# Kernel tuning notes

Measured on AMD Instinct MI355X. Metric: run time of the kernel, lower is better.

Reference implementation:

```python
import jax, jax.numpy as jnp
import numpy as np

N = 100000   # total nodes in batch
E = 1600000  # directed edges
G = 512      # graphs in batch
D_IN = 128
H = 128      # hidden_dim
L = 5        # num GIN layers
BN_EPS = 1e-5


def _bn(x, p):
    # p: [4, d] = (gamma, beta, running_mean, running_var); eval-mode batchnorm
    g, b, m, v = p[0], p[1], p[2], p[3]
    return (x - m) * jax.lax.rsqrt(v + BN_EPS) * g + b


def _mk_bn(k, d):
    k1, k2, k3, k4 = jax.random.split(k, 4)
    return jnp.stack([
        jax.random.uniform(k1, (d,), minval=0.8, maxval=1.2),
        0.1 * jax.random.normal(k2, (d,)),
        0.1 * jax.random.normal(k3, (d,)),
        jax.random.uniform(k4, (d,), minval=0.5, maxval=1.5),
    ])


def _mk_w(k, fi, fo):
    return jax.random.normal(k, (fi, fo)) * (2.0 / (fi + fo)) ** 0.5


def setup_inputs() -> dict:
    key = jax.random.key(0)
    ks = iter(jax.random.split(key, 64))
    nk = lambda: next(ks)

    x = jax.random.normal(nk(), (N, D_IN), dtype=jnp.float32)
    edge_index = jax.random.randint(nk(), (2, E), 0, N, dtype=jnp.int32)
    batch = jnp.sort(jax.random.randint(nk(), (N,), 0, G, dtype=jnp.int32))

    in_W = _mk_w(nk(), D_IN, H); in_b = jnp.zeros((H,)); in_bn = _mk_bn(nk(), H)

    W1, b1, bn1, W2, b2, bn2, W3, b3, nbn = [], [], [], [], [], [], [], [], []
    for _ in range(L):
        W1.append(_mk_w(nk(), H, 3 * H)); b1.append(jnp.zeros((3 * H,))); bn1.append(_mk_bn(nk(), 3 * H))
        W2.append(_mk_w(nk(), 3 * H, 2 * H)); b2.append(jnp.zeros((2 * H,))); bn2.append(_mk_bn(nk(), 2 * H))
        W3.append(_mk_w(nk(), 2 * H, H)); b3.append(jnp.zeros((H,)))
        nbn.append(_mk_bn(nk(), H))
    stk = lambda xs: jnp.stack(xs)
    eps_g = 0.1 * jax.random.normal(nk(), (L,))

    cls_W1 = _mk_w(nk(), 3 * H, H); cls_b1 = jnp.zeros((H,)); cls_bn1 = _mk_bn(nk(), H)
    cls_W2 = _mk_w(nk(), H, H // 2); cls_b2 = jnp.zeros((H // 2,)); cls_bn2 = _mk_bn(nk(), H // 2)
    fin_W = _mk_w(nk(), H // 2, 6); fin_b = jnp.zeros((6,))

    return {
        "x": x, "edge_index": edge_index, "batch": batch,
        "in_W": in_W, "in_b": in_b, "in_bn": in_bn,
        "W1": stk(W1), "b1": stk(b1), "bn1": stk(bn1),
        "W2": stk(W2), "b2": stk(b2), "bn2": stk(bn2),
        "W3": stk(W3), "b3": stk(b3), "eps_g": eps_g, "node_bn": stk(nbn),
        "cls_W1": cls_W1, "cls_b1": cls_b1, "cls_bn1": cls_bn1,
        "cls_W2": cls_W2, "cls_b2": cls_b2, "cls_bn2": cls_bn2,
        "fin_W": fin_W, "fin_b": fin_b,
    }


def reference(x, edge_index, batch, in_W, in_b, in_bn, W1, b1, bn1, W2, b2, bn2,
              W3, b3, eps_g, node_bn, cls_W1, cls_b1, cls_bn1, cls_W2, cls_b2,
              cls_bn2, fin_W, fin_b):
    src, dst = edge_index[0], edge_index[1]
    # input projection (dropout is identity in eval mode)
    h = jax.nn.relu(_bn(x @ in_W + in_b, in_bn))  # [N, H]

    for i in range(L):
        # GINConv: (1 + eps) * x + sum over in-neighbors, then MLP
        agg = jax.ops.segment_sum(h[src], dst, num_segments=N)  # [N, H]
        z = (1.0 + eps_g[i]) * h + agg
        z = jax.nn.relu(_bn(z @ W1[i] + b1[i], bn1[i]))
        z = jax.nn.relu(_bn(z @ W2[i] + b2[i], bn2[i]))
        z = z @ W3[i] + b3[i]
        # node-level BatchNorm + ReLU after conv
        z = jax.nn.relu(_bn(z, node_bn[i]))
        h = z if i == 0 else h + z  # residual for i > 0

    # multi-pool readout: add / mean / max over graphs
    s = jax.ops.segment_sum(h, batch, num_segments=G)          # [G, H]
    cnt = jax.ops.segment_sum(jnp.ones((N,), h.dtype), batch, num_segments=G)
    mean = s / jnp.maximum(cnt, 1.0)[:, None]
    mx = jax.ops.segment_max(h, batch, num_segments=G)
    mx = jnp.where(cnt[:, None] > 0, mx, 0.0)
    g = jnp.concatenate([s, mean, mx], axis=1)                 # [G, 3H]

    f = jax.nn.relu(_bn(g @ cls_W1 + cls_b1, cls_bn1))
    f = jax.nn.relu(_bn(f @ cls_W2 + cls_b2, cls_bn2))
    logits = f @ fin_W + fin_b                                  # [G, 6]
    return logits
```

## Files before the change

kernel.cpp:

```cpp
#include <hip/hip_runtime.h>
#include <hip/hip_bf16.h>

#define GLOBAL_AS __attribute__((address_space(1)))
#define LDS_AS    __attribute__((address_space(3)))

typedef __attribute__((ext_vector_type(4))) float  f32x4;
typedef __attribute__((ext_vector_type(8))) short  bf16x8;

static constexpr int   H      = 128;
static constexpr float BN_EPS = 1e-5f;

__device__ __forceinline__ float bf2f(ushort u) {
  union { unsigned u; float f; } x; x.u = ((unsigned)u) << 16; return x.f;
}
__device__ __forceinline__ ushort f2bf(float f) {
  union { float f; unsigned u; } x; x.f = f;
  unsigned r = x.u + 0x7fffu + ((x.u >> 16) & 1u);
  return (ushort)(r >> 16);
}

__device__ __forceinline__ void fold_pack_one(const float* __restrict__ W,
                                              const float* __restrict__ b,
                                              const float* __restrict__ bn,
                                              int K, int NOUT, int idx,
                                              ushort* __restrict__ Wp,
                                              float* __restrict__ bout) {
  int o = idx / K, k = idx - o * K;
  float scale = 1.0f, shift = 0.0f;
  if (bn != nullptr) {
    float g = bn[o], be = bn[NOUT + o], m = bn[2 * NOUT + o], v = bn[3 * NOUT + o];
    scale = g * rsqrtf(v + BN_EPS);
    shift = be - m * scale;
  }
  int gt = o >> 4, lr = o & 15, ks = k >> 5, lk = (k >> 3) & 3, e = k & 7;
  size_t pos = ((((size_t)gt * (K / 32) + ks) * 64) + lk * 16 + lr) * 8 + e;
  Wp[pos] = f2bf(W[(size_t)k * NOUT + o] * scale);
  if (k == 0) bout[o] = b[o] * scale + shift;
}

__device__ __forceinline__ void fold_f32_one(const float* __restrict__ W,
                                             const float* __restrict__ b,
                                             const float* __restrict__ bn,
                                             int K, int NOUT, int idx,
                                             float* __restrict__ Wt,
                                             float* __restrict__ bout) {
  int o = idx / K, k = idx - o * K;
  float scale = 1.0f, shift = 0.0f;
  if (bn != nullptr) {
    float g = bn[o], be = bn[NOUT + o], m = bn[2 * NOUT + o], v = bn[3 * NOUT + o];
    scale = g * rsqrtf(v + BN_EPS);
    shift = be - m * scale;
  }
  Wt[(size_t)o * K + k] = W[(size_t)k * NOUT + o] * scale;
  if (k == 0) bout[o] = b[o] * scale + shift;
}

__global__ __launch_bounds__(256) void fold_all_kernel(
    const float* __restrict__ in_W, const float* __restrict__ in_b, const float* __restrict__ in_bn,
    const float* __restrict__ W1, const float* __restrict__ b1, const float* __restrict__ bn1,
    const float* __restrict__ W2, const float* __restrict__ b2, const float* __restrict__ bn2,
    const float* __restrict__ W3, const float* __restrict__ b3, const float* __restrict__ nbn,
    const float* __restrict__ cW1, const float* __restrict__ cb1, const float* __restrict__ cbn1,
    const float* __restrict__ cW2, const float* __restrict__ cb2, const float* __restrict__ cbn2,
    const float* __restrict__ fW, const float* __restrict__ fb,
    ushort* __restrict__ wIn, float* __restrict__ bIn,
    ushort* __restrict__ w1f, float* __restrict__ b1f,
    ushort* __restrict__ w2f, float* __restrict__ b2f,
    ushort* __restrict__ w3f, float* __restrict__ b3f,
    float* __restrict__ cw1f, float* __restrict__ cb1f,
    float* __restrict__ cw2f, float* __restrict__ cb2f,
    float* __restrict__ cw3f, float* __restrict__ cb3f) {
  int idx = blockIdx.x * 256 + threadIdx.x;
  if (idx < 16384) {
    fold_pack_one(in_W, in_b, in_bn, 128, 128, idx, wIn, bIn);
    return;
  }
  idx -= 16384;
  if (idx < 5 * 180224) {
    int layer = idx / 180224;
    int r = idx - layer * 180224;
    if (r < 49152) {
      fold_pack_one(W1 + (size_t)layer * 49152, b1 + (size_t)layer * 384,
                    bn1 + (size_t)layer * 4 * 384, 128, 384, r,
                    w1f + (size_t)layer * 49152, b1f + (size_t)layer * 384);
    } else if (r < 147456) {
      fold_pack_one(W2 + (size_t)layer * 98304, b2 + (size_t)layer * 256,
                    bn2 + (size_t)layer * 4 * 256, 384, 256, r - 49152,
                    w2f + (size_t)layer * 98304, b2f + (size_t)layer * 256);
    } else {
      fold_pack_one(W3 + (size_t)layer * 32768, b3 + (size_t)layer * 128,
                    nbn + (size_t)layer * 4 * 128, 256, 128, r - 147456,
                    w3f + (size_t)layer * 32768, b3f + (size_t)layer * 128);
    }
    return;
  }
  idx -= 5 * 180224;
  if (idx < 49152) { fold_f32_one(cW1, cb1, cbn1, 384, 128, idx, cw1f, cb1f); return; }
  idx -= 49152;
  if (idx < 8192)  { fold_f32_one(cW2, cb2, cbn2, 128, 64, idx, cw2f, cb2f); return; }
  idx -= 8192;
  if (idx < 384)   { fold_f32_one(fW, fb, nullptr, 64, 6, idx, cw3f, cb3f); return; }
}

__global__ void cvt4_kernel(const float* __restrict__ x, ushort* __restrict__ xb, int n4) {
  int i = blockIdx.x * blockDim.x + threadIdx.x;
  if (i >= n4) return;
  float4 v = ((const float4*)x)[i];
  ushort4 o; o.x = f2bf(v.x); o.y = f2bf(v.y); o.z = f2bf(v.z); o.w = f2bf(v.w);
  ((ushort4*)xb)[i] = o;
}

__global__ void hist_kernel(const int* __restrict__ idx, int n, int* __restrict__ cnt) {
  int i = blockIdx.x * blockDim.x + threadIdx.x;
  if (i < n) atomicAdd(&cnt[idx[i]], 1);
}

__global__ void gbound_kernel(const int* __restrict__ batch, int N, int G,
                              int* __restrict__ gptr) {
  int i = blockIdx.x * blockDim.x + threadIdx.x;
  if (i >= N) return;
  int b = batch[i];
  int prev = (i == 0) ? -1 : batch[i - 1];
  for (int g = prev + 1; g <= b; ++g) gptr[g] = i;
  if (i == N - 1) for (int g = b + 1; g <= G; ++g) gptr[g] = N;
}

__global__ void block_sum_kernel(const int* __restrict__ v, int n, int* __restrict__ bsum) {
  __shared__ int s[256];
  int i = blockIdx.x * 256 + threadIdx.x;
  int x = (i < n) ? v[i] : 0;
  s[threadIdx.x] = x; __syncthreads();
  for (int off = 128; off > 0; off >>= 1) {
    if (threadIdx.x < (unsigned)off) s[threadIdx.x] += s[threadIdx.x + off];
    __syncthreads();
  }
  if (threadIdx.x == 0) bsum[blockIdx.x] = s[0];
}

__global__ void scan_block_kernel(int* __restrict__ bsum, int nb,
                                  int* __restrict__ last_out, int total) {
  __shared__ int s[256];
  __shared__ int carry;
  if (threadIdx.x == 0) carry = 0;
  __syncthreads();
  for (int base = 0; base < nb; base += 256) {
    int i = base + threadIdx.x;
    int x = (i < nb) ? bsum[i] : 0;
    s[threadIdx.x] = x; __syncthreads();
    for (int off = 1; off < 256; off <<= 1) {
      int add = (threadIdx.x >= (unsigned)off) ? s[threadIdx.x - off] : 0;
      __syncthreads();
      s[threadIdx.x] += add;
      __syncthreads();
    }
    if (i < nb) bsum[i] = carry + s[threadIdx.x] - x;
    __syncthreads();
    if (threadIdx.x == 0) carry += s[255];
    __syncthreads();
  }
  if (last_out && threadIdx.x == 0) *last_out = total;
}

__global__ void scan_final_kernel(const int* __restrict__ v, int n, const int* __restrict__ bsum,
                                  int* __restrict__ rowptr, int* __restrict__ cursor) {
  __shared__ int s[256];
  int i = blockIdx.x * 256 + threadIdx.x;
  int x = (i < n) ? v[i] : 0;
  s[threadIdx.x] = x; __syncthreads();
  for (int off = 1; off < 256; off <<= 1) {
    int add = (threadIdx.x >= (unsigned)off) ? s[threadIdx.x - off] : 0;
    __syncthreads();
    s[threadIdx.x] += add;
    __syncthreads();
  }
  if (i < n) {
    int excl = bsum[blockIdx.x] + s[threadIdx.x] - x;
    rowptr[i] = excl;
    if (cursor) cursor[i] = excl;
  }
}

__global__ __launch_bounds__(256) void scatter_part_kernel(
    const int* __restrict__ src, const int* __restrict__ dst, int E,
    int* __restrict__ cursor, int* __restrict__ col, int npp) {
  const int part  = blockIdx.x & 7;
  const int chunk = blockIdx.x >> 3;
  const int lo = part * npp, hi = lo + npp;
  const int i0 = chunk * 1024 + threadIdx.x * 4;
  if (i0 + 3 < E) {
    int4 d4 = *(const int4*)(dst + i0);
    if (d4.x >= lo && d4.x < hi) { int p = atomicAdd(&cursor[d4.x], 1); col[p] = src[i0 + 0]; }
    if (d4.y >= lo && d4.y < hi) { int p = atomicAdd(&cursor[d4.y], 1); col[p] = src[i0 + 1]; }
    if (d4.z >= lo && d4.z < hi) { int p = atomicAdd(&cursor[d4.z], 1); col[p] = src[i0 + 2]; }
    if (d4.w >= lo && d4.w < hi) { int p = atomicAdd(&cursor[d4.w], 1); col[p] = src[i0 + 3]; }
  } else {
    for (int u = 0; u < 4; ++u) {
      int i = i0 + u;
      if (i < E) {
        int d = dst[i];
        if (d >= lo && d < hi) { int p = atomicAdd(&cursor[d], 1); col[p] = src[i]; }
      }
    }
  }
}

__global__ __launch_bounds__(256) void agg_kernel(
    const ushort* __restrict__ hb,
    const int* __restrict__ rowptr, const int* __restrict__ col,
    const float* __restrict__ eps_g, int layer,
    ushort* __restrict__ z, int n) {
  int node = blockIdx.x * 4 + (threadIdx.x >> 6);
  if (node >= n) return;
  const int lane = threadIdx.x & 63;
  const int l16  = lane & 15;
  const int grp  = lane >> 4;
  const int s = rowptr[node], e = rowptr[node + 1];
  float a0 = 0.f, a1 = 0.f, a2 = 0.f, a3 = 0.f, a4 = 0.f, a5 = 0.f, a6 = 0.f, a7 = 0.f;
  const size_t co = (size_t)l16 * 8;
  int j = s + grp;
  for (; j + 12 < e; j += 16) {
    int i0 = col[j], i1 = col[j + 4], i2 = col[j + 8], i3 = col[j + 12];
    bf16x8 v0 = *(const bf16x8*)(hb + (size_t)i0 * H + co);
    bf16x8 v1 = *(const bf16x8*)(hb + (size_t)i1 * H + co);
    bf16x8 v2 = *(const bf16x8*)(hb + (size_t)i2 * H + co);
    bf16x8 v3 = *(const bf16x8*)(hb + (size_t)i3 * H + co);
    a0 += (bf2f((ushort)v0[0]) + bf2f((ushort)v1[0])) + (bf2f((ushort)v2[0]) + bf2f((ushort)v3[0]));
    a1 += (bf2f((ushort)v0[1]) + bf2f((ushort)v1[1])) + (bf2f((ushort)v2[1]) + bf2f((ushort)v3[1]));
    a2 += (bf2f((ushort)v0[2]) + bf2f((ushort)v1[2])) + (bf2f((ushort)v2[2]) + bf2f((ushort)v3[2]));
    a3 += (bf2f((ushort)v0[3]) + bf2f((ushort)v1[3])) + (bf2f((ushort)v2[3]) + bf2f((ushort)v3[3]));
    a4 += (bf2f((ushort)v0[4]) + bf2f((ushort)v1[4])) + (bf2f((ushort)v2[4]) + bf2f((ushort)v3[4]));
    a5 += (bf2f((ushort)v0[5]) + bf2f((ushort)v1[5])) + (bf2f((ushort)v2[5]) + bf2f((ushort)v3[5]));
    a6 += (bf2f((ushort)v0[6]) + bf2f((ushort)v1[6])) + (bf2f((ushort)v2[6]) + bf2f((ushort)v3[6]));
    a7 += (bf2f((ushort)v0[7]) + bf2f((ushort)v1[7])) + (bf2f((ushort)v2[7]) + bf2f((ushort)v3[7]));
  }
  for (; j + 4 < e; j += 8) {
    int i0 = col[j], i1 = col[j + 4];
    bf16x8 v0 = *(const bf16x8*)(hb + (size_t)i0 * H + co);
    bf16x8 v1 = *(const bf16x8*)(hb + (size_t)i1 * H + co);
    a0 += bf2f((ushort)v0[0]) + bf2f((ushort)v1[0]);
    a1 += bf2f((ushort)v0[1]) + bf2f((ushort)v1[1]);
    a2 += bf2f((ushort)v0[2]) + bf2f((ushort)v1[2]);
    a3 += bf2f((ushort)v0[3]) + bf2f((ushort)v1[3]);
    a4 += bf2f((ushort)v0[4]) + bf2f((ushort)v1[4]);
    a5 += bf2f((ushort)v0[5]) + bf2f((ushort)v1[5]);
    a6 += bf2f((ushort)v0[6]) + bf2f((ushort)v1[6]);
    a7 += bf2f((ushort)v0[7]) + bf2f((ushort)v1[7]);
  }
  if (j < e) {
    bf16x8 v0 = *(const bf16x8*)(hb + (size_t)col[j] * H + co);
    a0 += bf2f((ushort)v0[0]); a1 += bf2f((ushort)v0[1]);
    a2 += bf2f((ushort)v0[2]); a3 += bf2f((ushort)v0[3]);
    a4 += bf2f((ushort)v0[4]); a5 += bf2f((ushort)v0[5]);
    a6 += bf2f((ushort)v0[6]); a7 += bf2f((ushort)v0[7]);
  }
  a0 += __shfl_xor(a0, 16); a0 += __shfl_xor(a0, 32);
  a1 += __shfl_xor(a1, 16); a1 += __shfl_xor(a1, 32);
  a2 += __shfl_xor(a2, 16); a2 += __shfl_xor(a2, 32);
  a3 += __shfl_xor(a3, 16); a3 += __shfl_xor(a3, 32);
  a4 += __shfl_xor(a4, 16); a4 += __shfl_xor(a4, 32);
  a5 += __shfl_xor(a5, 16); a5 += __shfl_xor(a5, 32);
  a6 += __shfl_xor(a6, 16); a6 += __shfl_xor(a6, 32);
  a7 += __shfl_xor(a7, 16); a7 += __shfl_xor(a7, 32);
  float sx, sy;
  if      (grp == 0) { sx = a0; sy = a1; }
  else if (grp == 1) { sx = a2; sy = a3; }
  else if (grp == 2) { sx = a4; sy = a5; }
  else               { sx = a6; sy = a7; }
  const int c0 = l16 * 8 + grp * 2;
  float ep = 1.0f + eps_g[layer];
  ushort2 hs = *(const ushort2*)(hb + (size_t)node * H + c0);
  ushort2 o;
  o.x = f2bf(ep * bf2f(hs.x) + sx);
  o.y = f2bf(ep * bf2f(hs.y) + sy);
  *(ushort2*)(z + (size_t)node * H + c0) = o;
}

template<int K, int NOUT>
__global__ __launch_bounds__(256) void gemm_kernel(
    const ushort* __restrict__ A, const ushort* __restrict__ Wp,
    const float* __restrict__ bias,
    ushort* __restrict__ outb, float* __restrict__ hf) {
  constexpr int ROWB = 2 * K;
  __shared__ __align__(16) char lds[64 * ROWB];
  const int t = threadIdx.x;
  const long row0 = (long)blockIdx.x * 64;
  const char* Ab = (const char*)(A + (size_t)row0 * K);

  constexpr int ITERS = (64 * ROWB) / (256 * 16);
#pragma unroll
  for (int it = 0; it < ITERS; ++it) {
    int ob = (it * 256 + t) * 16;
    int r = ob / ROWB;
    int c = ob - r * ROWB;
    int sb = r * ROWB + (c ^ ((r & 7) << 4));
    __builtin_amdgcn_global_load_lds((const GLOBAL_AS void*)(Ab + sb),
                                     (LDS_AS void*)(lds + ob), 16, 0, 0);
  }
  __syncthreads();

  const int l  = t & 63;
  const int w  = t >> 6;
  const int lr = l & 15;
  const int lk = l >> 4;
  constexpr int CPW = NOUT / 4;
  constexpr int NCT = CPW / 16;

  for (int ct = 0; ct < NCT; ++ct) {
    const int colbase = w * CPW + ct * 16;
    const ushort* tb = Wp + ((size_t)(colbase >> 4) * (K / 32)) * 512;
    f32x4 acc[4] = {};
#pragma unroll
    for (int ks = 0; ks < K / 32; ++ks) {
      bf16x8 bfr = *(const bf16x8*)(tb + ks * 512 + l * 8);
#pragma unroll
      for (int rt = 0; rt < 4; ++rt) {
        const int rr = rt * 16 + lr;
        const int kb = ks * 64 + lk * 16;
        bf16x8 afr = *(const bf16x8*)(lds + rr * ROWB + (kb ^ ((rr & 7) << 4)));
        acc[rt] = __builtin_amdgcn_mfma_f32_16x16x32_bf16(bfr, afr, acc[rt], 0, 0, 0);
      }
    }
    const int c0 = colbase + lk * 4;
    const float b0 = bias[c0], b1 = bias[c0 + 1], b2 = bias[c0 + 2], b3 = bias[c0 + 3];
#pragma unroll
    for (int rt = 0; rt < 4; ++rt) {
      const long grow = row0 + rt * 16 + lr;
      float v0 = fmaxf(acc[rt][0] + b0, 0.f);
      float v1 = fmaxf(acc[rt][1] + b1, 0.f);
      float v2 = fmaxf(acc[rt][2] + b2, 0.f);
      float v3 = fmaxf(acc[rt][3] + b3, 0.f);
      *(float4*)(hf + grow * H + c0) = make_float4(v0, v1, v2, v3);
      ushort4 sv; sv.x = f2bf(v0); sv.y = f2bf(v1); sv.z = f2bf(v2); sv.w = f2bf(v3);
      *(ushort4*)(outb + grow * NOUT + c0) = sv;
    }
  }
}

template<int HMODE>
__global__ __launch_bounds__(256, 4) void mlp_fused_kernel(
    const ushort* __restrict__ zin,
    const ushort* __restrict__ w1, const float* __restrict__ bb1,
    const ushort* __restrict__ w2, const float* __restrict__ bb2,
    const ushort* __restrict__ w3, const float* __restrict__ bb3,
    ushort* __restrict__ hb, float* __restrict__ hf) {
  __shared__ __align__(16) char lds[40 * 1024];
  char* t1 = lds;
  char* zz = lds + 24 * 1024;
  char* t2 = lds + 24 * 1024;

  const int t = threadIdx.x;
  const long row0 = (long)blockIdx.x * 32;
  const char* Ab = (const char*)(zin + (size_t)row0 * 128);

#pragma unroll
  for (int it = 0; it < 2; ++it) {
    int ob = (it * 256 + t) * 16;
    int r = ob >> 8;
    int c = ob & 255;
    int sb = r * 256 + (c ^ ((r & 7) << 4));
    __builtin_amdgcn_global_load_lds((const GLOBAL_AS void*)(Ab + sb),
                                     (LDS_AS void*)(zz + ob), 16, 0, 0);
  }
  __syncthreads();

  const int l  = t & 63;
  const int w  = t >> 6;
  const int lr = l & 15;
  const int lk = l >> 4;

#pragma unroll
  for (int pass = 0; pass < 2; ++pass) {
    const int cb0 = w * 96 + pass * 48;
    f32x4 acc[3][2] = {};
#pragma unroll
    for (int ks = 0; ks < 4; ++ks) {
      bf16x8 afr[2];
#pragma unroll
      for (int rt = 0; rt < 2; ++rt) {
        const int rr = rt * 16 + lr;
        afr[rt] = *(const bf16x8*)(zz + rr * 256 + ((ks * 64 + lk * 16) ^ ((rr & 7) << 4)));
      }
#pragma unroll
      for (int ct = 0; ct < 3; ++ct) {
        bf16x8 bfr = *(const bf16x8*)(w1 + ((size_t)(cb0 / 16 + ct) * 4 + ks) * 512 + l * 8);
#pragma unroll
        for (int rt = 0; rt < 2; ++rt)
          acc[ct][rt] = __builtin_amdgcn_mfma_f32_16x16x32_bf16(bfr, afr[rt], acc[ct][rt], 0, 0, 0);
      }
    }
#pragma unroll
    for (int ct = 0; ct < 3; ++ct) {
      const int c0 = cb0 + ct * 16 + lk * 4;
      const float b0 = bb1[c0], b1 = bb1[c0 + 1], b2 = bb1[c0 + 2], b3 = bb1[c0 + 3];
#pragma unroll
      for (int rt = 0; rt < 2; ++rt) {
        const int rr = rt * 16 + lr;
        ushort4 sv;
        sv.x = f2bf(fmaxf(acc[ct][rt][0] + b0, 0.f));
        sv.y = f2bf(fmaxf(acc[ct][rt][1] + b1, 0.f));
        sv.z = f2bf(fmaxf(acc[ct][rt][2] + b2, 0.f));
        sv.w = f2bf(fmaxf(acc[ct][rt][3] + b3, 0.f));
        *(ushort4*)(t1 + rr * 768 + ((c0 * 2) ^ ((rr & 7) << 4))) = sv;
      }
    }
  }
  __syncthreads();

  {
    f32x4 acc[4][2] = {};
#pragma unroll
    for (int ks = 0; ks < 12; ++ks) {
      bf16x8 afr[2];
#pragma unroll
      for (int rt = 0; rt < 2; ++rt) {
        const int rr = rt * 16 + lr;
        afr[rt] = *(const bf16x8*)(t1 + rr * 768 + ((ks * 64 + lk * 16) ^ ((rr & 7) << 4)));
      }
#pragma unroll
      for (int ct = 0; ct < 4; ++ct) {
        bf16x8 bfr = *(const bf16x8*)(w2 + ((size_t)(w * 4 + ct) * 12 + ks) * 512 + l * 8);
#pragma unroll
        for (int rt = 0; rt < 2; ++rt)
          acc[ct][rt] = __builtin_amdgcn_mfma_f32_16x16x32_bf16(bfr, afr[rt], acc[ct][rt], 0, 0, 0);
      }
    }
    __syncthreads();
#pragma unroll
    for (int ct = 0; ct < 4; ++ct) {
      const int c0 = w * 64 + ct * 16 + lk * 4;
      const float b0 = bb2[c0], b1 = bb2[c0 + 1], b2 = bb2[c0 + 2], b3 = bb2[c0 + 3];
#pragma unroll
      for (int rt = 0; rt < 2; ++rt) {
        const int rr = rt * 16 + lr;
        ushort4 sv;
        sv.x = f2bf(fmaxf(acc[ct][rt][0] + b0, 0.f));
        sv.y = f2bf(fmaxf(acc[ct][rt][1] + b1, 0.f));
        sv.z = f2bf(fmaxf(acc[ct][rt][2] + b2, 0.f));
        sv.w = f2bf(fmaxf(acc[ct][rt][3] + b3, 0.f));
        *(ushort4*)(t2 + rr * 512 + ((c0 * 2) ^ ((rr & 7) << 4))) = sv;
      }
    }
  }
  __syncthreads();

  {
    f32x4 acc[2][2] = {};
#pragma unroll
    for (int ks = 0; ks < 8; ++ks) {
      bf16x8 afr[2];
#pragma unroll
      for (int rt = 0; rt < 2; ++rt) {
        const int rr = rt * 16 + lr;
        afr[rt] = *(const bf16x8*)(t2 + rr * 512 + ((ks * 64 + lk * 16) ^ ((rr & 7) << 4)));
      }
#pragma unroll
      for (int ct = 0; ct < 2; ++ct) {
        bf16x8 bfr = *(const bf16x8*)(w3 + ((size_t)(w * 2 + ct) * 8 + ks) * 512 + l * 8);
#pragma unroll
        for (int rt = 0; rt < 2; ++rt)
          acc[ct][rt] = __builtin_amdgcn_mfma_f32_16x16x32_bf16(bfr, afr[rt], acc[ct][rt], 0, 0, 0);
      }
    }
#pragma unroll
    for (int ct = 0; ct < 2; ++ct) {
      const int c0 = w * 32 + ct * 16 + lk * 4;
      const float b0 = bb3[c0], b1 = bb3[c0 + 1], b2 = bb3[c0 + 2], b3v = bb3[c0 + 3];
#pragma unroll
      for (int rt = 0; rt < 2; ++rt) {
        const long grow = row0 + rt * 16 + lr;
        float v0 = fmaxf(acc[ct][rt][0] + b0, 0.f);
        float v1 = fmaxf(acc[ct][rt][1] + b1, 0.f);
        float v2 = fmaxf(acc[ct][rt][2] + b2, 0.f);
        float v3 = fmaxf(acc[ct][rt][3] + b3v, 0.f);
        float4* hp = (float4*)(hf + grow * H + c0);
        if (HMODE == 2) {
          float4 o = *hp;
          v0 += o.x; v1 += o.y; v2 += o.z; v3 += o.w;
        }
        *hp = make_float4(v0, v1, v2, v3);
        ushort4 sv; sv.x = f2bf(v0); sv.y = f2bf(v1); sv.z = f2bf(v2); sv.w = f2bf(v3);
        *(ushort4*)(hb + grow * H + c0) = sv;
      }
    }
  }
}

__global__ __launch_bounds__(128) void readout_kernel(const float* __restrict__ hf,
                                                      const int* __restrict__ gptr,
                                                      float* __restrict__ g) {
  int gi = blockIdx.x, t = threadIdx.x;
  int s = gptr[gi], e = gptr[gi + 1];
  float sum = 0.f, mx = -INFINITY;
  for (int n = s; n < e; ++n) {
    float v = hf[(size_t)n * H + t];
    sum += v; mx = fmaxf(mx, v);
  }
  int cnt = e - s;
  g[gi * 384 + t]       = sum;
  g[gi * 384 + 128 + t] = sum / fmaxf((float)cnt, 1.f);
  g[gi * 384 + 256 + t] = (cnt > 0) ? mx : 0.f;
}

__global__ __launch_bounds__(128) void classifier_kernel(
    const float* __restrict__ g,
    const float* __restrict__ W1, const float* __restrict__ b1,
    const float* __restrict__ W2, const float* __restrict__ b2,
    const float* __restrict__ W3, const float* __restrict__ b3,
    float* __restrict__ out) {
  __shared__ float row[384];
  __shared__ float f1[128];
  __shared__ float f2s[64];
  int gi = blockIdx.x, t = threadIdx.x;
  for (int i = t; i < 384; i += 128) row[i] = g[gi * 384 + i];
  __syncthreads();
  float a = b1[t];
  for (int k = 0; k < 384; ++k) a += row[k] * W1[t * 384 + k];
  f1[t] = fmaxf(a, 0.f);
  __syncthreads();
  if (t < 64) {
    float a2 = b2[t];
    for (int k = 0; k < 128; ++k) a2 += f1[k] * W2[t * 128 + k];
    f2s[t] = fmaxf(a2, 0.f);
  }
  __syncthreads();
  if (t < 6) {
    float a3 = b3[t];
    for (int k = 0; k < 64; ++k) a3 += f2s[k] * W3[t * 64 + k];
    out[gi * 6 + t] = a3;
  }
}

extern "C" void kernel_launch(void* const* d_in, const int* in_sizes, int n_in,
                              void* d_out, int out_size, void* d_ws, size_t ws_size,
                              hipStream_t stream) {
  (void)n_in; (void)ws_size;
  const float* x     = (const float*)d_in[0];
  const int*   eidx  = (const int*)d_in[1];
  const int*   batch = (const int*)d_in[2];
  const float* in_W  = (const float*)d_in[3];
  const float* in_b  = (const float*)d_in[4];
  const float* in_bn = (const float*)d_in[5];
  const float* W1    = (const float*)d_in[6];
  const float* b1    = (const float*)d_in[7];
  const float* bn1   = (const float*)d_in[8];
  const float* W2    = (const float*)d_in[9];
  const float* b2    = (const float*)d_in[10];
  const float* bn2   = (const float*)d_in[11];
  const float* W3    = (const float*)d_in[12];
  const float* b3    = (const float*)d_in[13];
  const float* eps_g = (const float*)d_in[14];
  const float* nbn   = (const float*)d_in[15];
  const float* cW1   = (const float*)d_in[16];
  const float* cb1   = (const float*)d_in[17];
  const float* cbn1  = (const float*)d_in[18];
  const float* cW2   = (const float*)d_in[19];
  const float* cb2   = (const float*)d_in[20];
  const float* cbn2  = (const float*)d_in[21];
  const float* fW    = (const float*)d_in[22];
  const float* fb    = (const float*)d_in[23];

  const int N  = in_sizes[0] / 128;
  const int E  = in_sizes[1] / 2;
  const int G  = out_size / 6;
  const int Mp = ((N + 63) / 64) * 64;
  const int gblocks = Mp / 64;
  const int mblocks = Mp / 32;
  const int npp = (N + 7) / 8;
  const int nchunks = (E + 1023) / 1024;

  char* p = (char*)d_ws;
  auto alloc = [&](size_t bytes) -> char* {
    char* r = p; p += (bytes + 255) & ~(size_t)255; return r;
  };
  ushort* hb     = (ushort*)alloc((size_t)Mp * H * 2);
  ushort* zb     = (ushort*)alloc((size_t)Mp * H * 2);
  ushort* xb     = (ushort*)alloc((size_t)Mp * H * 2);
  float*  hf     = (float*)alloc((size_t)Mp * H * 4);
  int*    deg    = (int*)alloc((size_t)N * 4);
  int*    rowptr = (int*)alloc((size_t)(N + 1) * 4);
  int*    cursor = (int*)alloc((size_t)N * 4);
  int*    colx   = (int*)alloc((size_t)E * 4);
  int*    bsum   = (int*)alloc(4096);
  int*    gptr   = (int*)alloc((size_t)(G + 1) * 4);
  float*  gbuf   = (float*)alloc((size_t)G * 384 * 4);
  ushort* wIn    = (ushort*)alloc(128 * 128 * 2);
  float*  bIn    = (float*)alloc(128 * 4);
  ushort* w1f    = (ushort*)alloc((size_t)5 * 384 * 128 * 2);
  float*  b1f    = (float*)alloc((size_t)5 * 384 * 4);
  ushort* w2f    = (ushort*)alloc((size_t)5 * 256 * 384 * 2);
  float*  b2f    = (float*)alloc((size_t)5 * 256 * 4);
  ushort* w3f    = (ushort*)alloc((size_t)5 * 128 * 256 * 2);
  float*  b3f    = (float*)alloc((size_t)5 * 128 * 4);
  float*  cw1f   = (float*)alloc(128 * 384 * 4);
  float*  cb1f   = (float*)alloc(128 * 4);
  float*  cw2f   = (float*)alloc(64 * 128 * 4);
  float*  cb2f   = (float*)alloc(64 * 4);
  float*  cw3f   = (float*)alloc(6 * 64 * 4);
  float*  cb3f   = (float*)alloc(6 * 4);

  const int fold_total = 16384 + 5 * 180224 + 49152 + 8192 + 384;
  fold_all_kernel<<<(fold_total + 255) / 256, 256, 0, stream>>>(
      in_W, in_b, in_bn, W1, b1, bn1, W2, b2, bn2, W3, b3, nbn,
      cW1, cb1, cbn1, cW2, cb2, cbn2, fW, fb,
      wIn, bIn, w1f, b1f, w2f, b2f, w3f, b3f,
      cw1f, cb1f, cw2f, cb2f, cw3f, cb3f);

  cvt4_kernel<<<(N * 128 / 4 + 255) / 256, 256, 0, stream>>>(x, xb, N * 128 / 4);

  hipMemsetAsync(deg, 0, (size_t)N * 4, stream);
  hist_kernel<<<(E + 255) / 256, 256, 0, stream>>>(eidx + E, E, deg);
  gbound_kernel<<<(N + 255) / 256, 256, 0, stream>>>(batch, N, G, gptr);
  const int nb = (N + 255) / 256;
  block_sum_kernel<<<nb, 256, 0, stream>>>(deg, N, bsum);
  scan_block_kernel<<<1, 256, 0, stream>>>(bsum, nb, rowptr + N, E);
  scan_final_kernel<<<nb, 256, 0, stream>>>(deg, N, bsum, rowptr, cursor);
  scatter_part_kernel<<<nchunks * 8, 256, 0, stream>>>(eidx, eidx + E, E, cursor, colx, npp);

  gemm_kernel<128, 128><<<gblocks, 256, 0, stream>>>(xb, wIn, bIn, hb, hf);

  for (int i = 0; i < 5; ++i) {
    agg_kernel<<<(N + 3) / 4, 256, 0, stream>>>(hb, rowptr, colx, eps_g, i, zb, N);
    if (i == 0)
      mlp_fused_kernel<1><<<mblocks, 256, 0, stream>>>(
          zb, w1f + (size_t)i * 384 * 128, b1f + (size_t)i * 384,
          w2f + (size_t)i * 256 * 384, b2f + (size_t)i * 256,
          w3f + (size_t)i * 128 * 256, b3f + (size_t)i * 128, hb, hf);
    else
      mlp_fused_kernel<2><<<mblocks, 256, 0, stream>>>(
          zb, w1f + (size_t)i * 384 * 128, b1f + (size_t)i * 384,
          w2f + (size_t)i * 256 * 384, b2f + (size_t)i * 256,
          w3f + (size_t)i * 128 * 256, b3f + (size_t)i * 128, hb, hf);
  }

  readout_kernel<<<G, 128, 0, stream>>>(hf, gptr, gbuf);
  classifier_kernel<<<G, 128, 0, stream>>>(gbuf, cw1f, cb1f, cw2f, cb2f, cw3f, cb3f,
                                           (float*)d_out);
}
```

Baseline: 920.4 us.

## Enlarge fused MLP tile to 64 rows with 8 waves per block

The fused three-layer MLP kernel now processes 64 rows per block with 512 threads (8 waves) instead of 32 rows with 256 threads. Each wave covers a narrower slice of output columns but all four 16-row tiles, so every weight fragment loaded from global memory feeds four MFMAs instead of two. This halves per-row weight traffic. In exchange the block needs 64 KB of LDS, which limits residency per CU, and there are half as many blocks.

```diff
diff --git a/kernel.cpp b/kernel.cpp
--- a/kernel.cpp
+++ b/kernel.cpp
@@ -337,24 +337,24 @@
 }
 
 template<int HMODE>
-__global__ __launch_bounds__(256, 4) void mlp_fused_kernel(
+__global__ __launch_bounds__(512, 4) void mlp_fused_kernel(
     const ushort* __restrict__ zin,
     const ushort* __restrict__ w1, const float* __restrict__ bb1,
     const ushort* __restrict__ w2, const float* __restrict__ bb2,
     const ushort* __restrict__ w3, const float* __restrict__ bb3,
     ushort* __restrict__ hb, float* __restrict__ hf) {
-  __shared__ __align__(16) char lds[40 * 1024];
+  __shared__ __align__(16) char lds[64 * 1024];
   char* t1 = lds;
-  char* zz = lds + 24 * 1024;
-  char* t2 = lds + 24 * 1024;
+  char* zz = lds + 48 * 1024;
+  char* t2 = lds + 32 * 1024;
 
   const int t = threadIdx.x;
-  const long row0 = (long)blockIdx.x * 32;
+  const long row0 = (long)blockIdx.x * 64;
   const char* Ab = (const char*)(zin + (size_t)row0 * 128);
 
 #pragma unroll
   for (int it = 0; it < 2; ++it) {
-    int ob = (it * 256 + t) * 16;
+    int ob = (it * 512 + t) * 16;
     int r = ob >> 8;
     int c = ob & 255;
     int sb = r * 256 + (c ^ ((r & 7) << 4));
@@ -368,32 +368,30 @@
   const int lr = l & 15;
   const int lk = l >> 4;
 
-#pragma unroll
-  for (int pass = 0; pass < 2; ++pass) {
-    const int cb0 = w * 96 + pass * 48;
-    f32x4 acc[3][2] = {};
+  {
+    f32x4 acc[3][4] = {};
 #pragma unroll
     for (int ks = 0; ks < 4; ++ks) {
-      bf16x8 afr[2];
-#pragma unroll
-      for (int rt = 0; rt < 2; ++rt) {
+      bf16x8 afr[4];
+#pragma unroll
+      for (int rt = 0; rt < 4; ++rt) {
         const int rr = rt * 16 + lr;
         afr[rt] = *(const bf16x8*)(zz + rr * 256 + ((ks * 64 + lk * 16) ^ ((rr & 7) << 4)));
       }
 #pragma unroll
       for (int ct = 0; ct < 3; ++ct) {
-        bf16x8 bfr = *(const bf16x8*)(w1 + ((size_t)(cb0 / 16 + ct) * 4 + ks) * 512 + l * 8);
-#pragma unroll
-        for (int rt = 0; rt < 2; ++rt)
+        bf16x8 bfr = *(const bf16x8*)(w1 + ((size_t)(w * 3 + ct) * 4 + ks) * 512 + l * 8);
+#pragma unroll
+        for (int rt = 0; rt < 4; ++rt)
           acc[ct][rt] = __builtin_amdgcn_mfma_f32_16x16x32_bf16(bfr, afr[rt], acc[ct][rt], 0, 0, 0);
       }
     }
 #pragma unroll
     for (int ct = 0; ct < 3; ++ct) {
-      const int c0 = cb0 + ct * 16 + lk * 4;
+      const int c0 = w * 48 + ct * 16 + lk * 4;
       const float b0 = bb1[c0], b1 = bb1[c0 + 1], b2 = bb1[c0 + 2], b3 = bb1[c0 + 3];
 #pragma unroll
-      for (int rt = 0; rt < 2; ++rt) {
+      for (int rt = 0; rt < 4; ++rt) {
         const int rr = rt * 16 + lr;
         ushort4 sv;
         sv.x = f2bf(fmaxf(acc[ct][rt][0] + b0, 0.f));
@@ -407,30 +405,30 @@
   __syncthreads();
 
   {
-    f32x4 acc[4][2] = {};
+    f32x4 acc[2][4] = {};
 #pragma unroll
     for (int ks = 0; ks < 12; ++ks) {
-      bf16x8 afr[2];
-#pragma unroll
-      for (int rt = 0; rt < 2; ++rt) {
+      bf16x8 afr[4];
+#pragma unroll
+      for (int rt = 0; rt < 4; ++rt) {
         const int rr = rt * 16 + lr;
         afr[rt] = *(const bf16x8*)(t1 + rr * 768 + ((ks * 64 + lk * 16) ^ ((rr & 7) << 4)));
       }
 #pragma unroll
-      for (int ct = 0; ct < 4; ++ct) {
-        bf16x8 bfr = *(const bf16x8*)(w2 + ((size_t)(w * 4 + ct) * 12 + ks) * 512 + l * 8);
-#pragma unroll
-        for (int rt = 0; rt < 2; ++rt)
+      for (int ct = 0; ct < 2; ++ct) {
+        bf16x8 bfr = *(const bf16x8*)(w2 + ((size_t)(w * 2 + ct) * 12 + ks) * 512 + l * 8);
+#pragma unroll
+        for (int rt = 0; rt < 4; ++rt)
           acc[ct][rt] = __builtin_amdgcn_mfma_f32_16x16x32_bf16(bfr, afr[rt], acc[ct][rt], 0, 0, 0);
       }
     }
     __syncthreads();
 #pragma unroll
-    for (int ct = 0; ct < 4; ++ct) {
-      const int c0 = w * 64 + ct * 16 + lk * 4;
+    for (int ct = 0; ct < 2; ++ct) {
+      const int c0 = w * 32 + ct * 16 + lk * 4;
       const float b0 = bb2[c0], b1 = bb2[c0 + 1], b2 = bb2[c0 + 2], b3 = bb2[c0 + 3];
 #pragma unroll
-      for (int rt = 0; rt < 2; ++rt) {
+      for (int rt = 0; rt < 4; ++rt) {
         const int rr = rt * 16 + lr;
         ushort4 sv;
         sv.x = f2bf(fmaxf(acc[ct][rt][0] + b0, 0.f));
@@ -444,43 +442,37 @@
   __syncthreads();
 
   {
-    f32x4 acc[2][2] = {};
+    f32x4 acc[4] = {};
 #pragma unroll
     for (int ks = 0; ks < 8; ++ks) {
-      bf16x8 afr[2];
-#pragma unroll
-      for (int rt = 0; rt < 2; ++rt) {
+      bf16x8 afr[4];
+#pragma unroll
+      for (int rt = 0; rt < 4; ++rt) {
         const int rr = rt * 16 + lr;
         afr[rt] = *(const bf16x8*)(t2 + rr * 512 + ((ks * 64 + lk * 16) ^ ((rr & 7) << 4)));
       }
-#pragma unroll
-      for (int ct = 0; ct < 2; ++ct) {
-        bf16x8 bfr = *(const bf16x8*)(w3 + ((size_t)(w * 2 + ct) * 8 + ks) * 512 + l * 8);
-#pragma unroll
-        for (int rt = 0; rt < 2; ++rt)
-          acc[ct][rt] = __builtin_amdgcn_mfma_f32_16x16x32_bf16(bfr, afr[rt], acc[ct][rt], 0, 0, 0);
-      }
-    }
-#pragma unroll
-    for (int ct = 0; ct < 2; ++ct) {
-      const int c0 = w * 32 + ct * 16 + lk * 4;
-      const float b0 = bb3[c0], b1 = bb3[c0 + 1], b2 = bb3[c0 + 2], b3v = bb3[c0 + 3];
-#pragma unroll
-      for (int rt = 0; rt < 2; ++rt) {
-        const long grow = row0 + rt * 16 + lr;
-        float v0 = fmaxf(acc[ct][rt][0] + b0, 0.f);
-        float v1 = fmaxf(acc[ct][rt][1] + b1, 0.f);
-        float v2 = fmaxf(acc[ct][rt][2] + b2, 0.f);
-        float v3 = fmaxf(acc[ct][rt][3] + b3v, 0.f);
-        float4* hp = (float4*)(hf + grow * H + c0);
-        if (HMODE == 2) {
-          float4 o = *hp;
-          v0 += o.x; v1 += o.y; v2 += o.z; v3 += o.w;
-        }
-        *hp = make_float4(v0, v1, v2, v3);
-        ushort4 sv; sv.x = f2bf(v0); sv.y = f2bf(v1); sv.z = f2bf(v2); sv.w = f2bf(v3);
-        *(ushort4*)(hb + grow * H + c0) = sv;
-      }
+      bf16x8 bfr = *(const bf16x8*)(w3 + ((size_t)w * 8 + ks) * 512 + l * 8);
+#pragma unroll
+      for (int rt = 0; rt < 4; ++rt)
+        acc[rt] = __builtin_amdgcn_mfma_f32_16x16x32_bf16(bfr, afr[rt], acc[rt], 0, 0, 0);
+    }
+    const int c0 = w * 16 + lk * 4;
+    const float b0 = bb3[c0], b1 = bb3[c0 + 1], b2 = bb3[c0 + 2], b3v = bb3[c0 + 3];
+#pragma unroll
+    for (int rt = 0; rt < 4; ++rt) {
+      const long grow = row0 + rt * 16 + lr;
+      float v0 = fmaxf(acc[rt][0] + b0, 0.f);
+      float v1 = fmaxf(acc[rt][1] + b1, 0.f);
+      float v2 = fmaxf(acc[rt][2] + b2, 0.f);
+      float v3 = fmaxf(acc[rt][3] + b3v, 0.f);
+      float4* hp = (float4*)(hf + grow * H + c0);
+      if (HMODE == 2) {
+        float4 o = *hp;
+        v0 += o.x; v1 += o.y; v2 += o.z; v3 += o.w;
+      }
+      *hp = make_float4(v0, v1, v2, v3);
+      ushort4 sv; sv.x = f2bf(v0); sv.y = f2bf(v1); sv.z = f2bf(v2); sv.w = f2bf(v3);
+      *(ushort4*)(hb + grow * H + c0) = sv;
     }
   }
 }
@@ -564,7 +556,6 @@
   const int G  = out_size / 6;
   const int Mp = ((N + 63) / 64) * 64;
   const int gblocks = Mp / 64;
-  const int mblocks = Mp / 32;
   const int npp = (N + 7) / 8;
   const int nchunks = (E + 1023) / 1024;
 
@@ -621,12 +612,12 @@
   for (int i = 0; i < 5; ++i) {
     agg_kernel<<<(N + 3) / 4, 256, 0, stream>>>(hb, rowptr, colx, eps_g, i, zb, N);
     if (i == 0)
-      mlp_fused_kernel<1><<<mblocks, 256, 0, stream>>>(
+      mlp_fused_kernel<1><<<gblocks, 512, 0, stream>>>(
           zb, w1f + (size_t)i * 384 * 128, b1f + (size_t)i * 384,
           w2f + (size_t)i * 256 * 384, b2f + (size_t)i * 256,
           w3f + (size_t)i * 128 * 256, b3f + (size_t)i * 128, hb, hf);
     else
-      mlp_fused_kernel<2><<<mblocks, 256, 0, stream>>>(
+      mlp_fused_kernel<2><<<gblocks, 512, 0, stream>>>(
           zb, w1f + (size_t)i * 384 * 128, b1f + (size_t)i * 384,
           w2f + (size_t)i * 256 * 384, b2f + (size_t)i * 256,
           w3f + (size_t)i * 128 * 256, b3f + (size_t)i * 128, hb, hf);
```

Measured after the change: 876.1 us. 4.8% less time.
